# Performance work log

Measured on AMD Instinct MI355X. Metric: run time of the kernel, lower is better.

The kernel has to match this reference:

```python
import jax, jax.numpy as jnp
import numpy as np

B, T, T_OUT, D = 32, 2048, 512, 256
LN_EPS = 1e-5


def _ragged_adaptive_avg_pool(mu_mel, mel_lengths, target_lens):
    """Vectorized per-sample adaptive_avg_pool1d over ragged lengths.

    For sample b with input length L=mel_lengths[b] and output length
    O=target_lens[b], output bin j averages input frames
    [floor(j*L/O), ceil((j+1)*L/O)). Bins j >= O are zero (pad_sequence).
    Returns [B, T_OUT, D].
    """
    j = jnp.arange(T_OUT, dtype=jnp.int32)[None, :, None]   # [1, T_OUT, 1]
    t = jnp.arange(T, dtype=jnp.int32)[None, None, :]       # [1, 1, T]
    L = mel_lengths.astype(jnp.int32)[:, None, None]        # [B, 1, 1]
    O = target_lens.astype(jnp.int32)[:, None, None]        # [B, 1, 1]
    start = (j * L) // O                                     # [B, T_OUT, 1]
    end = ((j + 1) * L + O - 1) // O                         # ceil division
    valid = j < O
    w = ((t >= start) & (t < end) & valid).astype(mu_mel.dtype)  # [B, T_OUT, T]
    cnt = jnp.maximum(end - start, 1).astype(mu_mel.dtype)
    w = w / cnt
    return jnp.einsum('bjt,btd->bjd', w, mu_mel)             # [B, T_OUT, D]


def setup_inputs() -> dict:
    key = jax.random.key(0)
    k1, k2, k3, k4 = jax.random.split(key, 4)
    mu_mel = jax.random.normal(k1, (B, T, D), dtype=jnp.float32)
    mel_lengths = jax.random.randint(k2, (B,), T // 2, T + 1, dtype=jnp.int32)
    target_lens = jax.random.randint(k3, (B,), T_OUT // 2, T_OUT + 1, dtype=jnp.int32)
    conv_w = jax.random.normal(k4, (D, D), dtype=jnp.float32) * (1.0 / np.sqrt(D))
    gamma = jnp.ones((D,), dtype=jnp.float32)
    beta = jnp.zeros((D,), dtype=jnp.float32)
    return {"mu_mel": mu_mel, "mel_lengths": mel_lengths,
            "target_lens": target_lens, "conv_w": conv_w,
            "gamma": gamma, "beta": beta}


def reference(mu_mel, mel_lengths, target_lens, conv_w, gamma, beta):
    # ragged adaptive avg pool + pad into [B, T_OUT, D]; torch wraps this in
    # no_grad, so stop_gradient mirrors that.
    pooled = jax.lax.stop_gradient(
        _ragged_adaptive_avg_pool(mu_mel, mel_lengths, target_lens))
    # 1x1 Conv1d (no bias) == per-position matmul, then exact GELU
    h = jax.nn.gelu(jnp.einsum('bjd,ed->bje', pooled, conv_w), approximate=False)
    # LayerNorm over D (applied to padded positions too, as in torch)
    mean = jnp.mean(h, axis=-1, keepdims=True)
    var = jnp.mean(jnp.square(h - mean), axis=-1, keepdims=True)
    return (h - mean) * jax.lax.rsqrt(var + LN_EPS) * gamma + beta
```

## Files before the change

kernel.cpp:

```cpp
#include <hip/hip_runtime.h>

#define NB 32
#define NT 2048
#define TOUT 512
#define ND 256
#define TILE_M 16
#define BLK_J 32
#define LDA 264
#define LDH 264

typedef __attribute__((ext_vector_type(4))) float f32x4;
typedef __attribute__((ext_vector_type(8))) short bf16x8;
typedef __attribute__((ext_vector_type(4))) unsigned short u16x4;

__device__ __forceinline__ unsigned short f2b(float f) {
    unsigned int u = __builtin_bit_cast(unsigned int, f);
    return (unsigned short)((u + 0x7FFFu + ((u >> 16) & 1u)) >> 16);
}

__device__ __forceinline__ float gelu_exact(float x) {
    return 0.5f * x * (1.0f + erff(x * 0.70710678118654752440f));
}

template <int K>
__device__ __forceinline__ f32x4 sumK(const float* p) {
    f32x4 v[K];
    #pragma unroll
    for (int t = 0; t < K; ++t)
        v[t] = *reinterpret_cast<const f32x4*>(p + (size_t)t * ND);
    f32x4 s = v[0];
    #pragma unroll
    for (int t = 1; t < K; ++t) s += v[t];
    return s;
}

__global__ __launch_bounds__(512)
void cvt_w_kernel(const float* __restrict__ wf, unsigned short* __restrict__ wbF) {
    const int gid = blockIdx.x * 512 + (int)threadIdx.x;
    const int l   = gid & 63;
    const int kk  = (gid >> 6) & 7;
    const int et  = gid >> 9;
    const int e   = et * 16 + (l & 15);
    const int k   = kk * 32 + (l >> 4) * 8;
    f32x4 a = *reinterpret_cast<const f32x4*>(wf + e * ND + k);
    f32x4 c = *reinterpret_cast<const f32x4*>(wf + e * ND + k + 4);
    u16x4 p0, p1;
    p0.x = f2b(a.x); p0.y = f2b(a.y); p0.z = f2b(a.z); p0.w = f2b(a.w);
    p1.x = f2b(c.x); p1.y = f2b(c.y); p1.z = f2b(c.z); p1.w = f2b(c.w);
    *reinterpret_cast<u16x4*>(wbF + (size_t)gid * 8)     = p0;
    *reinterpret_cast<u16x4*>(wbF + (size_t)gid * 8 + 4) = p1;
}

__global__ __launch_bounds__(512, 2)
void fused_kernel(const float* __restrict__ mu,
                  const int* __restrict__ lens,
                  const int* __restrict__ olens,
                  const unsigned short* __restrict__ wbF,
                  const float* __restrict__ gamma,
                  const float* __restrict__ beta,
                  float* __restrict__ out)
{
    __shared__ unsigned short a_lds[2][TILE_M * LDA];
    __shared__ float h_lds[2][TILE_M * LDH];

    const int b    = blockIdx.x;
    const int j0   = blockIdx.y * BLK_J;
    const int tid  = (int)threadIdx.x;
    const int lane = tid & 63;
    const int wv   = tid >> 6;
    const int r    = lane & 15;
    const int kg   = lane >> 4;

    bf16x8 wreg[8][2];
    #pragma unroll
    for (int kk = 0; kk < 8; ++kk)
        #pragma unroll
        for (int p = 0; p < 2; ++p) {
            const int et = wv * 2 + p;
            wreg[kk][p] = *reinterpret_cast<const bf16x8*>(
                wbF + (size_t)((et * 8 + kk) * 64 + lane) * 8);
        }

    const int L = lens[b];
    const int O = olens[b];

    #pragma unroll
    for (int i = 0; i < 4; ++i) {
        const int m = wv + i * 8;
        const int j = j0 + m;
        f32x4 s = {0.f, 0.f, 0.f, 0.f};
        if (j < O) {
            const int st  = (j * L) / O;
            const int en  = ((j + 1) * L + O - 1) / O;
            const int cnt = en - st;
            const float* p = mu + (size_t)(b * NT + st) * ND + lane * 4;
            switch (cnt) {
                case 2: s = sumK<2>(p); break;
                case 3: s = sumK<3>(p); break;
                case 4: s = sumK<4>(p); break;
                case 5: s = sumK<5>(p); break;
                case 6: s = sumK<6>(p); break;
                case 7: s = sumK<7>(p); break;
                case 8: s = sumK<8>(p); break;
                case 9: s = sumK<9>(p); break;
                default:
                    for (int t = 0; t < cnt; ++t)
                        s += *reinterpret_cast<const f32x4*>(p + (size_t)t * ND);
                    break;
            }
            s *= 1.0f / (float)cnt;
        }
        u16x4 q;
        q.x = f2b(s.x); q.y = f2b(s.y); q.z = f2b(s.z); q.w = f2b(s.w);
        *reinterpret_cast<u16x4*>(&a_lds[m >> 4][(m & 15) * LDA + lane * 4]) = q;
    }
    __syncthreads();

    #pragma unroll
    for (int t = 0; t < 2; ++t) {
        f32x4 acc[2];
        acc[0] = (f32x4){0.f, 0.f, 0.f, 0.f};
        acc[1] = (f32x4){0.f, 0.f, 0.f, 0.f};
        #pragma unroll
        for (int kk = 0; kk < 8; ++kk) {
            const int k0 = kk * 32 + kg * 8;
            bf16x8 af = *reinterpret_cast<const bf16x8*>(&a_lds[t][r * LDA + k0]);
            acc[0] = __builtin_amdgcn_mfma_f32_16x16x32_bf16(af, wreg[kk][0], acc[0], 0, 0, 0);
            acc[1] = __builtin_amdgcn_mfma_f32_16x16x32_bf16(af, wreg[kk][1], acc[1], 0, 0, 0);
        }
        #pragma unroll
        for (int p = 0; p < 2; ++p) {
            const int col = wv * 32 + p * 16 + r;
            #pragma unroll
            for (int q = 0; q < 4; ++q)
                h_lds[t][(kg * 4 + q) * LDH + col] = gelu_exact(acc[p][q]);
        }
    }
    __syncthreads();

    const f32x4 g4 = *reinterpret_cast<const f32x4*>(&gamma[lane * 4]);
    const f32x4 b4 = *reinterpret_cast<const f32x4*>(&beta[lane * 4]);
    #pragma unroll
    for (int i = 0; i < 4; ++i) {
        const int m = wv + i * 8;
        f32x4 v = *reinterpret_cast<const f32x4*>(&h_lds[m >> 4][(m & 15) * LDH + lane * 4]);
        float s  = v.x + v.y + v.z + v.w;
        float sq = v.x * v.x + v.y * v.y + v.z * v.z + v.w * v.w;
        #pragma unroll
        for (int off = 32; off > 0; off >>= 1) {
            s  += __shfl_xor(s, off, 64);
            sq += __shfl_xor(sq, off, 64);
        }
        const float mean = s * (1.0f / 256.0f);
        const float var  = sq * (1.0f / 256.0f) - mean * mean;
        const float rs   = rsqrtf(var + 1e-5f);
        f32x4 o = (v - mean) * rs * g4 + b4;
        *reinterpret_cast<f32x4*>(&out[((size_t)(b * TOUT) + j0 + m) * ND + lane * 4]) = o;
    }
}

__global__ __launch_bounds__(256, 4)
void fused_fallback(const float* __restrict__ mu,
                    const int* __restrict__ lens,
                    const int* __restrict__ olens,
                    const float* __restrict__ wf,
                    const float* __restrict__ gamma,
                    const float* __restrict__ beta,
                    float* __restrict__ out)
{
    __shared__ unsigned short a_lds[TILE_M * LDA];
    __shared__ float h_lds[TILE_M * LDH];

    const int b    = blockIdx.x;
    const int j0   = blockIdx.y * TILE_M;
    const int tid  = (int)threadIdx.x;
    const int lane = tid & 63;
    const int wv   = tid >> 6;
    const int L = lens[b];
    const int O = olens[b];

    for (int m = wv; m < TILE_M; m += 4) {
        const int j = j0 + m;
        f32x4 acc = {0.f, 0.f, 0.f, 0.f};
        if (j < O) {
            const int s = (j * L) / O;
            const int e = ((j + 1) * L + O - 1) / O;
            const float* src = mu + (size_t)(b * NT + s) * ND + lane * 4;
            for (int t = s; t < e; ++t) {
                acc += *reinterpret_cast<const f32x4*>(src);
                src += ND;
            }
            acc *= (1.0f / (float)(e - s));
        }
        u16x4 p;
        p.x = f2b(acc.x); p.y = f2b(acc.y); p.z = f2b(acc.z); p.w = f2b(acc.w);
        *reinterpret_cast<u16x4*>(&a_lds[m * LDA + lane * 4]) = p;
    }
    __syncthreads();

    const int r  = lane & 15;
    const int kg = lane >> 4;
    const int e0 = wv * 64;
    f32x4 acc[4];
    #pragma unroll
    for (int c = 0; c < 4; ++c) acc[c] = (f32x4){0.f, 0.f, 0.f, 0.f};
    #pragma unroll
    for (int kk = 0; kk < 8; ++kk) {
        const int k0 = kk * 32 + kg * 8;
        bf16x8 af = *reinterpret_cast<const bf16x8*>(&a_lds[r * LDA + k0]);
        #pragma unroll
        for (int ct = 0; ct < 4; ++ct) {
            const int e = e0 + ct * 16 + r;
            f32x4 w0 = *reinterpret_cast<const f32x4*>(&wf[e * ND + k0]);
            f32x4 w1 = *reinterpret_cast<const f32x4*>(&wf[e * ND + k0 + 4]);
            union { bf16x8 v; unsigned short u[8]; } cv;
            cv.u[0] = f2b(w0.x); cv.u[1] = f2b(w0.y);
            cv.u[2] = f2b(w0.z); cv.u[3] = f2b(w0.w);
            cv.u[4] = f2b(w1.x); cv.u[5] = f2b(w1.y);
            cv.u[6] = f2b(w1.z); cv.u[7] = f2b(w1.w);
            acc[ct] = __builtin_amdgcn_mfma_f32_16x16x32_bf16(af, cv.v, acc[ct], 0, 0, 0);
        }
    }
    #pragma unroll
    for (int ct = 0; ct < 4; ++ct) {
        const int col  = e0 + ct * 16 + r;
        const int row0 = kg * 4;
        #pragma unroll
        for (int q = 0; q < 4; ++q)
            h_lds[(row0 + q) * LDH + col] = gelu_exact(acc[ct][q]);
    }
    __syncthreads();
    const f32x4 g4 = *reinterpret_cast<const f32x4*>(&gamma[lane * 4]);
    const f32x4 b4 = *reinterpret_cast<const f32x4*>(&beta[lane * 4]);
    #pragma unroll
    for (int i = 0; i < 4; ++i) {
        const int m = wv + i * 4;
        f32x4 v = *reinterpret_cast<const f32x4*>(&h_lds[m * LDH + lane * 4]);
        float s  = v.x + v.y + v.z + v.w;
        float sq = v.x * v.x + v.y * v.y + v.z * v.z + v.w * v.w;
        #pragma unroll
        for (int off = 32; off > 0; off >>= 1) {
            s  += __shfl_xor(s, off, 64);
            sq += __shfl_xor(sq, off, 64);
        }
        const float mean = s * (1.0f / 256.0f);
        const float var  = sq * (1.0f / 256.0f) - mean * mean;
        const float rs   = rsqrtf(var + 1e-5f);
        f32x4 o = (v - mean) * rs * g4 + b4;
        *reinterpret_cast<f32x4*>(&out[((size_t)(b * TOUT) + j0 + m) * ND + lane * 4]) = o;
    }
}

extern "C" void kernel_launch(void* const* d_in, const int* in_sizes, int n_in,
                              void* d_out, int out_size, void* d_ws, size_t ws_size,
                              hipStream_t stream) {
    const float* mu    = (const float*)d_in[0];
    const int*   lens  = (const int*)d_in[1];
    const int*   olens = (const int*)d_in[2];
    const float* wf    = (const float*)d_in[3];
    const float* gamma = (const float*)d_in[4];
    const float* beta  = (const float*)d_in[5];
    float* out = (float*)d_out;

    const size_t need = (size_t)ND * ND * sizeof(unsigned short);

    if (ws_size >= need) {
        unsigned short* wbF = (unsigned short*)d_ws;
        cvt_w_kernel<<<dim3(16), dim3(512), 0, stream>>>(wf, wbF);
        fused_kernel<<<dim3(NB, TOUT / BLK_J), dim3(512), 0, stream>>>(
            mu, lens, olens, wbF, gamma, beta, out);
    } else {
        fused_fallback<<<dim3(NB, TOUT / TILE_M), dim3(256), 0, stream>>>(
            mu, lens, olens, wf, gamma, beta, out);
    }
}
```

Measured before the change: 26.81 us.

## Software-pipeline pooling and MFMA across two row tiles, use tanh GELU

The kernel now splits the 32-row block into two 16-row halves. The second half's pooling loads run while the first half's MFMA and GELU execute, and the first half's LayerNorm overlaps the second half's MFMA. The second-half pooling replaces the switch on bin count with branchless clamped loads of eight frames plus an optional ninth, which raises memory-level parallelism. Exact erf GELU is swapped for a tanh-form approximation built from __expf, which cuts transcendental cost but changes numerics slightly.

```diff
diff --git a/kernel.cpp b/kernel.cpp
--- a/kernel.cpp
+++ b/kernel.cpp
@@ -16,6 +16,14 @@
 __device__ __forceinline__ unsigned short f2b(float f) {
     unsigned int u = __builtin_bit_cast(unsigned int, f);
     return (unsigned short)((u + 0x7FFFu + ((u >> 16) & 1u)) >> 16);
+}
+
+__device__ __forceinline__ float gelu_fast(float x) {
+    float x2 = x * x;
+    float p  = x * fmaf(x2, 0.044715f, 1.0f);
+    float a  = fminf(1.5957691216f * p, 80.0f);
+    float e  = __expf(a);
+    return x * __fdividef(e, e + 1.0f);
 }
 
 __device__ __forceinline__ float gelu_exact(float x) {
@@ -83,9 +91,11 @@
 
     const int L = lens[b];
     const int O = olens[b];
-
-    #pragma unroll
-    for (int i = 0; i < 4; ++i) {
+    const f32x4 g4 = *reinterpret_cast<const f32x4*>(&gamma[lane * 4]);
+    const f32x4 b4 = *reinterpret_cast<const f32x4*>(&beta[lane * 4]);
+
+    #pragma unroll
+    for (int i = 0; i < 2; ++i) {
         const int m = wv + i * 8;
         const int j = j0 + m;
         f32x4 s = {0.f, 0.f, 0.f, 0.f};
@@ -112,19 +122,51 @@
         }
         u16x4 q;
         q.x = f2b(s.x); q.y = f2b(s.y); q.z = f2b(s.z); q.w = f2b(s.w);
-        *reinterpret_cast<u16x4*>(&a_lds[m >> 4][(m & 15) * LDA + lane * 4]) = q;
-    }
-    __syncthreads();
-
-    #pragma unroll
-    for (int t = 0; t < 2; ++t) {
+        *reinterpret_cast<u16x4*>(&a_lds[0][m * LDA + lane * 4]) = q;
+    }
+    __syncthreads();
+
+    #pragma unroll
+    for (int i = 0; i < 2; ++i) {
+        const int m1 = wv + i * 8;
+        const int j  = j0 + 16 + m1;
+        f32x4 s = {0.f, 0.f, 0.f, 0.f};
+        int cnt = 0; float inv = 0.f;
+        const float* bp = mu + (size_t)b * NT * ND + lane * 4;
+        if (j < O) {
+            const int st = (j * L) / O;
+            const int en = ((j + 1) * L + O - 1) / O;
+            cnt = en - st;
+            inv = 1.0f / (float)cnt;
+            bp  = mu + (size_t)(b * NT + st) * ND + lane * 4;
+        }
+        const int cm1 = (cnt > 0) ? (cnt - 1) : 0;
+        f32x4 v[8];
+        #pragma unroll
+        for (int t = 0; t < 8; ++t) {
+            const int tc = (t < cm1) ? t : cm1;
+            v[t] = *reinterpret_cast<const f32x4*>(bp + (size_t)tc * ND);
+        }
+        #pragma unroll
+        for (int t = 0; t < 8; ++t) {
+            const float w = (t < cnt) ? inv : 0.f;
+            s += v[t] * w;
+        }
+        if (cnt == 9)
+            s += *reinterpret_cast<const f32x4*>(bp + (size_t)8 * ND) * inv;
+        u16x4 q;
+        q.x = f2b(s.x); q.y = f2b(s.y); q.z = f2b(s.z); q.w = f2b(s.w);
+        *reinterpret_cast<u16x4*>(&a_lds[1][m1 * LDA + lane * 4]) = q;
+    }
+
+    {
         f32x4 acc[2];
         acc[0] = (f32x4){0.f, 0.f, 0.f, 0.f};
         acc[1] = (f32x4){0.f, 0.f, 0.f, 0.f};
         #pragma unroll
         for (int kk = 0; kk < 8; ++kk) {
             const int k0 = kk * 32 + kg * 8;
-            bf16x8 af = *reinterpret_cast<const bf16x8*>(&a_lds[t][r * LDA + k0]);
+            bf16x8 af = *reinterpret_cast<const bf16x8*>(&a_lds[0][r * LDA + k0]);
             acc[0] = __builtin_amdgcn_mfma_f32_16x16x32_bf16(af, wreg[kk][0], acc[0], 0, 0, 0);
             acc[1] = __builtin_amdgcn_mfma_f32_16x16x32_bf16(af, wreg[kk][1], acc[1], 0, 0, 0);
         }
@@ -133,17 +175,35 @@
             const int col = wv * 32 + p * 16 + r;
             #pragma unroll
             for (int q = 0; q < 4; ++q)
-                h_lds[t][(kg * 4 + q) * LDH + col] = gelu_exact(acc[p][q]);
-        }
-    }
-    __syncthreads();
-
-    const f32x4 g4 = *reinterpret_cast<const f32x4*>(&gamma[lane * 4]);
-    const f32x4 b4 = *reinterpret_cast<const f32x4*>(&beta[lane * 4]);
-    #pragma unroll
-    for (int i = 0; i < 4; ++i) {
+                h_lds[0][(kg * 4 + q) * LDH + col] = gelu_fast(acc[p][q]);
+        }
+    }
+    __syncthreads();
+
+    {
+        f32x4 acc[2];
+        acc[0] = (f32x4){0.f, 0.f, 0.f, 0.f};
+        acc[1] = (f32x4){0.f, 0.f, 0.f, 0.f};
+        #pragma unroll
+        for (int kk = 0; kk < 8; ++kk) {
+            const int k0 = kk * 32 + kg * 8;
+            bf16x8 af = *reinterpret_cast<const bf16x8*>(&a_lds[1][r * LDA + k0]);
+            acc[0] = __builtin_amdgcn_mfma_f32_16x16x32_bf16(af, wreg[kk][0], acc[0], 0, 0, 0);
+            acc[1] = __builtin_amdgcn_mfma_f32_16x16x32_bf16(af, wreg[kk][1], acc[1], 0, 0, 0);
+        }
+        #pragma unroll
+        for (int p = 0; p < 2; ++p) {
+            const int col = wv * 32 + p * 16 + r;
+            #pragma unroll
+            for (int q = 0; q < 4; ++q)
+                h_lds[1][(kg * 4 + q) * LDH + col] = gelu_fast(acc[p][q]);
+        }
+    }
+
+    #pragma unroll
+    for (int i = 0; i < 2; ++i) {
         const int m = wv + i * 8;
-        f32x4 v = *reinterpret_cast<const f32x4*>(&h_lds[m >> 4][(m & 15) * LDH + lane * 4]);
+        f32x4 v = *reinterpret_cast<const f32x4*>(&h_lds[0][m * LDH + lane * 4]);
         float s  = v.x + v.y + v.z + v.w;
         float sq = v.x * v.x + v.y * v.y + v.z * v.z + v.w * v.w;
         #pragma unroll
@@ -156,6 +216,25 @@
         const float rs   = rsqrtf(var + 1e-5f);
         f32x4 o = (v - mean) * rs * g4 + b4;
         *reinterpret_cast<f32x4*>(&out[((size_t)(b * TOUT) + j0 + m) * ND + lane * 4]) = o;
+    }
+    __syncthreads();
+
+    #pragma unroll
+    for (int i = 0; i < 2; ++i) {
+        const int m = wv + i * 8;
+        f32x4 v = *reinterpret_cast<const f32x4*>(&h_lds[1][m * LDH + lane * 4]);
+        float s  = v.x + v.y + v.z + v.w;
+        float sq = v.x * v.x + v.y * v.y + v.z * v.z + v.w * v.w;
+        #pragma unroll
+        for (int off = 32; off > 0; off >>= 1) {
+            s  += __shfl_xor(s, off, 64);
+            sq += __shfl_xor(sq, off, 64);
+        }
+        const float mean = s * (1.0f / 256.0f);
+        const float var  = sq * (1.0f / 256.0f) - mean * mean;
+        const float rs   = rsqrtf(var + 1e-5f);
+        f32x4 o = (v - mean) * rs * g4 + b4;
+        *reinterpret_cast<f32x4*>(&out[((size_t)(b * TOUT) + j0 + 16 + m) * ND + lane * 4]) = o;
     }
 }
 
```

New measurement: 30.37 us. 1.13x slower.
